# Kernel optimization log

Hardware: AMD Instinct MI355X
Metric: run time of the kernel (lower is better)

Reference implementation:

```python
import jax, jax.numpy as jnp
import numpy as np


def _relative_position_index(S):
    # Faithful to the torch buffer construction, computed once with numpy (static).
    coords = np.stack(np.meshgrid(np.arange(S), np.arange(S), indexing='ij'))  # (2,S,S)
    coords = coords.reshape(2, -1)                                             # (2,N)
    rel = coords[:, :, None] - coords[:, None, :]                              # (2,N,N)
    rel = rel.transpose(1, 2, 0).astype(np.int64)                              # (N,N,2)
    rel[:, :, 0] += S - 1
    rel[:, :, 1] += S - 1
    rel[:, :, 0] *= 2 * S - 1
    idx = rel.sum(-1)
    idx = idx[::-1, ::-1].copy()  # flipud(fliplr(...))
    return idx                    # (N,N) int64 in [0, (2S-1)^2)


def setup_inputs() -> dict:
    key = jax.random.key(0)
    ks = jax.random.split(key, 6)
    B, S, C, NH = 8, 32, 512, 16
    x = jax.random.normal(ks[0], (B, S, S, C), dtype=jnp.float32)
    qkv_w = jax.random.normal(ks[1], (3 * C, C), dtype=jnp.float32) * 0.02
    qkv_b = jax.random.normal(ks[2], (3 * C,), dtype=jnp.float32) * 0.02
    rpb = jax.random.normal(ks[3], (NH, 2 * S - 1, 2 * S - 1), dtype=jnp.float32) * 0.02
    proj_w = jax.random.normal(ks[4], (C, C), dtype=jnp.float32) * 0.02
    proj_b = jax.random.normal(ks[5], (C,), dtype=jnp.float32) * 0.02
    return {"x": x, "qkv_w": qkv_w, "qkv_b": qkv_b, "rpb": rpb,
            "proj_w": proj_w, "proj_b": proj_b}


def reference(x, qkv_w, qkv_b, rpb, proj_w, proj_b):
    B, H, W, C = x.shape
    N = H * W
    num_heads = rpb.shape[0]
    head_dim = C // num_heads
    scale = head_dim ** (-0.5)
    S = H

    idx = _relative_position_index(S)  # static numpy (N,N)

    qkv = x.reshape(B, N, C) @ qkv_w.T + qkv_b            # (B,N,3C)
    qkv = qkv.reshape(B, N, 3, num_heads, head_dim)
    qkv = jnp.transpose(qkv, (2, 0, 3, 1, 4))             # (3,B,h,N,d)
    q, k, v = qkv[0], qkv[1], qkv[2]

    attn = jnp.einsum('bhnd,bhmd->bhnm', q * scale, k)    # (B,h,N,N)
    # gather relative position bias: (h,(2S-1)^2)[:, idx] -> (h,N,N)
    bias = rpb.reshape(num_heads, -1)[:, idx]
    attn = jax.nn.softmax(attn + bias[None], axis=-1)

    out = jnp.einsum('bhnm,bhmd->bhnd', attn, v)          # (B,h,N,d)
    out = jnp.transpose(out, (0, 2, 1, 3)).reshape(B, H, W, C)
    return out @ proj_w.T + proj_b
```

## Files before the change

kernel.cpp:

```cpp
#include <hip/hip_runtime.h>

typedef __bf16 bf16x8 __attribute__((ext_vector_type(8)));
typedef float f32x4 __attribute__((ext_vector_type(4)));
typedef unsigned short u16;
typedef unsigned int u32;

__device__ __forceinline__ float bf2f(u16 v) {
    union { unsigned u; float f; } x; x.u = ((unsigned)v) << 16; return x.f;
}
__device__ __forceinline__ u16 f2bf(float f) {
    union { float f; unsigned u; } x; x.f = f;
    unsigned r = x.u + 0x7fffu + ((x.u >> 16) & 1u);
    return (u16)(r >> 16);
}

__device__ __forceinline__ bool probe_is_f32(const void* xp) {
    const unsigned* p = (const unsigned*)xp;
    int hits = 0;
#pragma unroll
    for (int i = 0; i < 32; i++) {
        const unsigned e = (p[i] >> 7) & 0xffu;
        hits += (e >= 0x90u) ? 1 : 0;
    }
    return hits > 3;
}

__device__ __forceinline__ float ld1(const void* p, size_t i, bool isf32) {
    return isf32 ? ((const float*)p)[i] : bf2f(((const u16*)p)[i]);
}

__device__ __forceinline__ void gl2lds16(const void* g, void* l) {
    __builtin_amdgcn_global_load_lds(
        (const __attribute__((address_space(1))) u32*)g,
        (__attribute__((address_space(3))) u32*)l, 16, 0, 0);
}

__global__ __launch_bounds__(256)
void convert_inputs(const void* __restrict__ x, const void* __restrict__ qw,
                    const void* __restrict__ qb, const void* __restrict__ pw,
                    const void* __restrict__ pb, const void* __restrict__ rp,
                    u16* __restrict__ xbf, u16* __restrict__ qwbf,
                    u16* __restrict__ qbbf, u16* __restrict__ pwbf,
                    u16* __restrict__ pbbf, float* __restrict__ rpl2e)
{
    const bool isf32 = probe_is_f32(x);
    const int gid = blockIdx.x * 256 + threadIdx.x;
    const int gsz = gridDim.x * 256;

    struct Seg { const void* s; u16* d; int n; };
    const Seg segs[5] = {{x, xbf, 4194304}, {qw, qwbf, 786432}, {pw, pwbf, 262144},
                         {qb, qbbf, 1536}, {pb, pbbf, 512}};
    for (int t = 0; t < 5; t++) {
        const int n4 = segs[t].n >> 2;
        if (isf32) {
            const f32x4* s = (const f32x4*)segs[t].s;
            for (int i = gid; i < n4; i += gsz) {
                f32x4 v = s[i];
                ushort4 o;
                o.x = f2bf(v[0]); o.y = f2bf(v[1]); o.z = f2bf(v[2]); o.w = f2bf(v[3]);
                *(ushort4*)(segs[t].d + i * 4) = o;
            }
        } else {
            const ushort4* s = (const ushort4*)segs[t].s;
            for (int i = gid; i < n4; i += gsz) *(ushort4*)(segs[t].d + i * 4) = s[i];
        }
    }
    for (int i = gid; i < 63504; i += gsz)
        rpl2e[i] = ld1(rp, i, isf32) * 1.4426950408889634f;
}

template<int MODE, int BM>
__global__ __launch_bounds__(256, 2)
void gemm_bt(const u16* __restrict__ A, const u16* __restrict__ W,
             const u16* __restrict__ bias, void* __restrict__ out,
             u16* __restrict__ q_out, u16* __restrict__ k_out, u16* __restrict__ v_out,
             const void* __restrict__ probe, int Nout, int K)
{
    __shared__ __align__(16) u16 As[BM * 32];
    __shared__ __align__(16) u16 Ws[128 * 32];
    constexpr int RW = BM / 32;

    const int tid  = threadIdx.x;
    const int lane = tid & 63;
    const int wave = tid >> 6;
    const int quad = lane >> 4;
    const int l16  = lane & 15;
    const int m0 = blockIdx.y * BM;
    const int n0 = blockIdx.x * 128;
    const int wm = (wave >> 1) * (BM / 2);
    const int wn = (wave & 1) * 64;

    f32x4 acc[RW][4] = {};

    for (int k0 = 0; k0 < K; k0 += 32) {
        __syncthreads();
        {
            const u16* g = A + (size_t)(m0 + wave * 16 + (lane >> 2)) * K + k0 + (lane & 3) * 8;
            u16* l = As + wave * 16 * 32;
            for (int p = 0; p < BM / 64; p++) gl2lds16(g + (size_t)p * 64 * K, l + p * 64 * 32);
        }
        {
            const u16* g = W + (size_t)(n0 + wave * 16 + (lane >> 2)) * K + k0 + (lane & 3) * 8;
            u16* l = Ws + wave * 16 * 32;
            for (int p = 0; p < 2; p++) gl2lds16(g + (size_t)p * 64 * K, l + p * 64 * 32);
        }
        __syncthreads();

        bf16x8 af[RW], wf[4];
        for (int i = 0; i < RW; i++)
            af[i] = *(const bf16x8*)(As + (wm + i * 16 + l16) * 32 + quad * 8);
        for (int j = 0; j < 4; j++)
            wf[j] = *(const bf16x8*)(Ws + (wn + j * 16 + l16) * 32 + quad * 8);
        for (int i = 0; i < RW; i++)
            for (int j = 0; j < 4; j++)
                acc[i][j] = __builtin_amdgcn_mfma_f32_16x16x32_bf16(af[i], wf[j], acc[i][j], 0, 0, 0);
    }

    const bool isf32 = (MODE == 0) ? probe_is_f32(probe) : false;
    for (int j = 0; j < 4; j++) {
        const int col = n0 + wn + j * 16 + l16;
        const float bv = bf2f(bias[col]);
        if (MODE == 0) {
            for (int i = 0; i < RW; i++) {
                const int rbase = m0 + wm + i * 16 + quad * 4;
                for (int r = 0; r < 4; r++) {
                    const float val = acc[i][j][r] + bv;
                    if (isf32) ((float*)out)[(size_t)(rbase + r) * Nout + col] = val;
                    else       ((u16*)out)[(size_t)(rbase + r) * Nout + col]  = f2bf(val);
                }
            }
        } else {
            const int which = col >> 9;
            const int h = (col >> 5) & 15;
            const int c = col & 31;
            if (which == 2) {
                for (int i = 0; i < RW; i++) {
                    const int row = m0 + wm + i * 16 + quad * 4;
                    const int bi = row >> 10, t0 = row & 1023;
                    ushort4 pk;
                    pk.x = f2bf(acc[i][j][0] + bv); pk.y = f2bf(acc[i][j][1] + bv);
                    pk.z = f2bf(acc[i][j][2] + bv); pk.w = f2bf(acc[i][j][3] + bv);
                    *(ushort4*)(v_out + (((size_t)(bi * 16 + h)) * 32 + c) * 1024 + t0) = pk;
                }
            } else {
                u16* dst = which ? k_out : q_out;
                for (int i = 0; i < RW; i++) {
                    const int rbase = m0 + wm + i * 16 + quad * 4;
                    for (int r = 0; r < 4; r++) {
                        const int row = rbase + r;
                        const int bi = row >> 10, t = row & 1023;
                        dst[(((size_t)(bi * 16 + h)) * 1024 + t) * 32 + c] = f2bf(acc[i][j][r] + bv);
                    }
                }
            }
        }
    }
}

__global__ __launch_bounds__(256, 2)
void attn(const u16* __restrict__ q, const u16* __restrict__ k,
          const u16* __restrict__ vt, const float* __restrict__ rpl2e,
          u16* __restrict__ o)
{
    __shared__ __align__(16) u16 Qs[128 * 40];
    __shared__ __align__(16) u16 Ks[2][64 * 40];
    __shared__ __align__(16) u16 Vt[2][32 * 72];
    __shared__ __align__(16) u16 Ps[4][16 * 72];
    __shared__ float biasS[35 * 63];

    const int tid  = threadIdx.x;
    const int lane = tid & 63;
    const int wave = tid >> 6;
    const int quad = lane >> 4;
    const int l16  = lane & 15;

    const int qt = blockIdx.x;
    const int h  = blockIdx.y;
    const int b  = blockIdx.z;
    const int n0 = qt * 128;
    const size_t base = ((size_t)(b * 16 + h)) * 32768;

    {
        const int row = tid >> 2, seg = (tid & 3) * 8;
        for (int p = 0; p < 2; p++)
            *(uint4*)(Qs + (p * 64 + row) * 40 + seg) =
                *(const uint4*)(q + base + (size_t)(n0 + p * 64 + row) * 32 + seg);
    }
    {
        const int row0 = 28 - 4 * qt;
        for (int idx = tid; idx < 2205; idx += 256)
            biasS[idx] = rpl2e[(size_t)h * 3969 + (size_t)(row0 + idx / 63) * 63 + idx % 63];
    }
    uint4 kreg = *(const uint4*)(k + base + (size_t)(tid >> 2) * 32 + (tid & 3) * 8);
    uint4 vreg = *(const uint4*)(vt + base + (size_t)(tid >> 3) * 1024 + (tid & 7) * 8);
    *(uint4*)(Ks[0] + (tid >> 2) * 40 + (tid & 3) * 8) = kreg;
    *(uint4*)(Vt[0] + (tid >> 3) * 72 + (tid & 7) * 8) = vreg;
    __syncthreads();

    bf16x8 qf[2];
    for (int g = 0; g < 2; g++)
        qf[g] = *(const bf16x8*)(Qs + (g * 64 + wave * 16 + l16) * 40 + quad * 8);

    bf16x8 ones;
    for (int i = 0; i < 8; i++) ones[i] = (__bf16)1.0f;

    f32x4 o_acc[2][3] = {};
    const int bn = (wave & 1) * 16 + l16;
    const float SC = 0.25503485724582146f;
    u16* pw = Ps[wave];

    for (int kt = 0; kt < 16; kt++) {
        const int cur = kt & 1;
        if (kt < 15) {
            const int mn = (kt + 1) * 64;
            kreg = *(const uint4*)(k + base + (size_t)(mn + (tid >> 2)) * 32 + (tid & 3) * 8);
            vreg = *(const uint4*)(vt + base + (size_t)(tid >> 3) * 1024 + mn + (tid & 7) * 8);
        }

        bf16x8 kf[4];
        for (int j = 0; j < 4; j++)
            kf[j] = *(const bf16x8*)(Ks[cur] + (j * 16 + l16) * 40 + quad * 8);

        for (int g = 0; g < 2; g++) {
            f32x4 s4[4];
            const f32x4 zero = {};
            for (int j = 0; j < 4; j++)
                s4[j] = __builtin_amdgcn_mfma_f32_16x16x32_bf16(kf[j], qf[g], zero, 0, 0, 0);

            const int rbase = 2 * kt - (wave >> 1) - 2 * g + 3;
            for (int j = 0; j < 4; j++) {
                const float* brow = biasS + (rbase + (j >> 1)) * 63
                                   + ((j & 1) * 16 + quad * 4) - bn + 31;
                ushort4 pk;
                u16* pks = (u16*)&pk;
                for (int r = 0; r < 4; r++) {
                    const float pv = __builtin_amdgcn_exp2f(s4[j][r] * SC + brow[r]);
                    union { __bf16 b; u16 u; } cv; cv.b = (__bf16)pv;
                    pks[r] = cv.u;
                }
                *(ushort4*)(pw + l16 * 72 + j * 16 + quad * 4) = pk;
            }

            for (int kc = 0; kc < 2; kc++) {
                const bf16x8 pa = *(const bf16x8*)(pw + l16 * 72 + kc * 32 + quad * 8);
                for (int ct = 0; ct < 2; ct++) {
                    const bf16x8 vf = *(const bf16x8*)(Vt[cur] + (ct * 16 + l16) * 72 + kc * 32 + quad * 8);
                    o_acc[g][ct] = __builtin_amdgcn_mfma_f32_16x16x32_bf16(pa, vf, o_acc[g][ct], 0, 0, 0);
                }
                o_acc[g][2] = __builtin_amdgcn_mfma_f32_16x16x32_bf16(pa, ones, o_acc[g][2], 0, 0, 0);
            }
        }

        if (kt < 15) {
            *(uint4*)(Ks[cur ^ 1] + (tid >> 2) * 40 + (tid & 3) * 8) = kreg;
            *(uint4*)(Vt[cur ^ 1] + (tid >> 3) * 72 + (tid & 7) * 8) = vreg;
        }
        __syncthreads();
    }

    for (int g = 0; g < 2; g++)
        for (int r = 0; r < 4; r++) {
            const float inv = __builtin_amdgcn_rcpf(o_acc[g][2][r]);
            const int n = n0 + g * 64 + wave * 16 + quad * 4 + r;
            u16* orow = o + ((size_t)b * 1024 + n) * 512 + h * 32;
            orow[l16]      = f2bf(o_acc[g][0][r] * inv);
            orow[16 + l16] = f2bf(o_acc[g][1][r] * inv);
        }
}

extern "C" void kernel_launch(void* const* d_in, const int* in_sizes, int n_in,
                              void* d_out, int out_size, void* d_ws, size_t ws_size,
                              hipStream_t stream) {
    const void* x      = d_in[0];
    const void* qkv_w  = d_in[1];
    const void* qkv_b  = d_in[2];
    const void* rpb    = d_in[3];
    const void* proj_w = d_in[4];
    const void* proj_b = d_in[5];

    u16* ws    = (u16*)d_ws;
    u16* kb    = ws;
    u16* vb    = ws + 4194304;
    u16* xbf   = ws + 8388608;
    u16* ao    = xbf;
    u16* qwbf  = ws + 12582912;
    u16* pwbf  = ws + 13369344;
    u16* qbbf  = ws + 13631488;
    u16* pbbf  = ws + 13633024;
    float* rpl2e = (float*)(ws + 13633536);
    u16* qb    = (u16*)d_out;

    convert_inputs<<<1024, 256, 0, stream>>>(x, qkv_w, qkv_b, proj_w, proj_b, rpb,
                                             xbf, qwbf, qbbf, pwbf, pbbf, rpl2e);

    dim3 g1(1536 / 128, 8192 / 128);
    gemm_bt<1, 128><<<g1, 256, 0, stream>>>(xbf, qwbf, qbbf, nullptr, qb, kb, vb, x, 1536, 512);

    dim3 g2(8, 16, 8);
    attn<<<g2, 256, 0, stream>>>(qb, kb, vb, rpl2e, ao);

    dim3 g3(512 / 128, 8192 / 64);
    gemm_bt<0, 64><<<g3, 256, 0, stream>>>(ao, pwbf, pbbf, d_out, nullptr, nullptr, nullptr, x, 512, 512);
}
```

Before: 161.6 us.

## Swap QKV GEMM operands for vectorized Q/K stores; load Q directly into registers

The QKV projection GEMM now takes the weight matrix as its row operand and the tokens as its column operand. Each lane's four accumulator rows then hold consecutive head-dim channels, so Q and K can be written as packed ushort4 stores, while V becomes scattered scalar stores. The attention kernel drops the Q shared-memory tile and loads Q fragments straight from global memory into registers. It also raises the launch-bounds occupancy hint from 2 to 4 blocks, which trades register budget for more resident waves.

Result: faster. 156.8 us (-3.0%).

```diff
diff --git a/kernel.cpp b/kernel.cpp
--- a/kernel.cpp
+++ b/kernel.cpp
@@ -116,11 +116,11 @@
                 acc[i][j] = __builtin_amdgcn_mfma_f32_16x16x32_bf16(af[i], wf[j], acc[i][j], 0, 0, 0);
     }
 
-    const bool isf32 = (MODE == 0) ? probe_is_f32(probe) : false;
-    for (int j = 0; j < 4; j++) {
-        const int col = n0 + wn + j * 16 + l16;
-        const float bv = bf2f(bias[col]);
-        if (MODE == 0) {
+    if (MODE == 0) {
+        const bool isf32 = probe_is_f32(probe);
+        for (int j = 0; j < 4; j++) {
+            const int col = n0 + wn + j * 16 + l16;
+            const float bv = bf2f(bias[col]);
             for (int i = 0; i < RW; i++) {
                 const int rbase = m0 + wm + i * 16 + quad * 4;
                 for (int r = 0; r < 4; r++) {
@@ -129,40 +129,44 @@
                     else       ((u16*)out)[(size_t)(rbase + r) * Nout + col]  = f2bf(val);
                 }
             }
-        } else {
-            const int which = col >> 9;
-            const int h = (col >> 5) & 15;
-            const int c = col & 31;
-            if (which == 2) {
-                for (int i = 0; i < RW; i++) {
-                    const int row = m0 + wm + i * 16 + quad * 4;
-                    const int bi = row >> 10, t0 = row & 1023;
+        }
+    } else {
+        const int which = m0 >> 9;
+        float bv[RW][4];
+        for (int i = 0; i < RW; i++) {
+            const int row4 = m0 + wm + i * 16 + quad * 4;
+            for (int r = 0; r < 4; r++) bv[i][r] = bf2f(bias[row4 + r]);
+        }
+        for (int j = 0; j < 4; j++) {
+            const int tok = n0 + wn + j * 16 + l16;
+            const int bi = tok >> 10, t = tok & 1023;
+            for (int i = 0; i < RW; i++) {
+                const int row4 = m0 + wm + i * 16 + quad * 4;
+                const int h = (row4 >> 5) & 15;
+                const int c = row4 & 31;
+                if (which == 2) {
+                    for (int r = 0; r < 4; r++)
+                        v_out[((size_t)(bi * 16 + h) * 32 + c + r) * 1024 + t] =
+                            f2bf(acc[i][j][r] + bv[i][r]);
+                } else {
+                    u16* dst = which ? k_out : q_out;
                     ushort4 pk;
-                    pk.x = f2bf(acc[i][j][0] + bv); pk.y = f2bf(acc[i][j][1] + bv);
-                    pk.z = f2bf(acc[i][j][2] + bv); pk.w = f2bf(acc[i][j][3] + bv);
-                    *(ushort4*)(v_out + (((size_t)(bi * 16 + h)) * 32 + c) * 1024 + t0) = pk;
+                    pk.x = f2bf(acc[i][j][0] + bv[i][0]);
+                    pk.y = f2bf(acc[i][j][1] + bv[i][1]);
+                    pk.z = f2bf(acc[i][j][2] + bv[i][2]);
+                    pk.w = f2bf(acc[i][j][3] + bv[i][3]);
+                    *(ushort4*)(dst + ((size_t)(bi * 16 + h) * 1024 + t) * 32 + c) = pk;
                 }
-            } else {
-                u16* dst = which ? k_out : q_out;
-                for (int i = 0; i < RW; i++) {
-                    const int rbase = m0 + wm + i * 16 + quad * 4;
-                    for (int r = 0; r < 4; r++) {
-                        const int row = rbase + r;
-                        const int bi = row >> 10, t = row & 1023;
-                        dst[(((size_t)(bi * 16 + h)) * 1024 + t) * 32 + c] = f2bf(acc[i][j][r] + bv);
-                    }
-                }
-            }
-        }
-    }
-}
-
-__global__ __launch_bounds__(256, 2)
+            }
+        }
+    }
+}
+
+__global__ __launch_bounds__(256, 4)
 void attn(const u16* __restrict__ q, const u16* __restrict__ k,
           const u16* __restrict__ vt, const float* __restrict__ rpl2e,
           u16* __restrict__ o)
 {
-    __shared__ __align__(16) u16 Qs[128 * 40];
     __shared__ __align__(16) u16 Ks[2][64 * 40];
     __shared__ __align__(16) u16 Vt[2][32 * 72];
     __shared__ __align__(16) u16 Ps[4][16 * 72];
@@ -181,12 +185,6 @@
     const size_t base = ((size_t)(b * 16 + h)) * 32768;
 
     {
-        const int row = tid >> 2, seg = (tid & 3) * 8;
-        for (int p = 0; p < 2; p++)
-            *(uint4*)(Qs + (p * 64 + row) * 40 + seg) =
-                *(const uint4*)(q + base + (size_t)(n0 + p * 64 + row) * 32 + seg);
-    }
-    {
         const int row0 = 28 - 4 * qt;
         for (int idx = tid; idx < 2205; idx += 256)
             biasS[idx] = rpl2e[(size_t)h * 3969 + (size_t)(row0 + idx / 63) * 63 + idx % 63];
@@ -195,11 +193,14 @@
     uint4 vreg = *(const uint4*)(vt + base + (size_t)(tid >> 3) * 1024 + (tid & 7) * 8);
     *(uint4*)(Ks[0] + (tid >> 2) * 40 + (tid & 3) * 8) = kreg;
     *(uint4*)(Vt[0] + (tid >> 3) * 72 + (tid & 7) * 8) = vreg;
+
+    bf16x8 qf[2];
+    for (int g = 0; g < 2; g++) {
+        union { uint4 u; bf16x8 f; } cv;
+        cv.u = *(const uint4*)(q + base + (size_t)(n0 + g * 64 + wave * 16 + l16) * 32 + quad * 8);
+        qf[g] = cv.f;
+    }
     __syncthreads();
-
-    bf16x8 qf[2];
-    for (int g = 0; g < 2; g++)
-        qf[g] = *(const bf16x8*)(Qs + (g * 64 + wave * 16 + l16) * 40 + quad * 8);
 
     bf16x8 ones;
     for (int i = 0; i < 8; i++) ones[i] = (__bf16)1.0f;
@@ -293,8 +294,8 @@
     convert_inputs<<<1024, 256, 0, stream>>>(x, qkv_w, qkv_b, proj_w, proj_b, rpb,
                                              xbf, qwbf, qbbf, pwbf, pbbf, rpl2e);
 
-    dim3 g1(1536 / 128, 8192 / 128);
-    gemm_bt<1, 128><<<g1, 256, 0, stream>>>(xbf, qwbf, qbbf, nullptr, qb, kb, vb, x, 1536, 512);
+    dim3 g1(8192 / 128, 1536 / 128);
+    gemm_bt<1, 128><<<g1, 256, 0, stream>>>(qwbf, xbf, qbbf, nullptr, qb, kb, vb, x, 8192, 512);
 
     dim3 g2(8, 16, 8);
     attn<<<g2, 256, 0, stream>>>(qb, kb, vb, rpl2e, ao);
```
